# Kernel tuning notes

Hardware: AMD Instinct MI355X
Metric: run time of the kernel (lower is better)

Reference implementation:

```python
import jax, jax.numpy as jnp
import numpy as np

B, S, D = 4, 2048, 1024
LN_EPS = 1e-5
NEG_INF = -1e9


def _layernorm(x, gamma, beta):
    mu = jnp.mean(x, axis=-1, keepdims=True)
    var = jnp.var(x, axis=-1, keepdims=True)
    return (x - mu) * jax.lax.rsqrt(var + LN_EPS) * gamma + beta


def setup_inputs() -> dict:
    key = jax.random.key(0)
    k1, k2, k3, k4 = jax.random.split(key, 4)
    context = jax.random.normal(k1, (B, S, D), dtype=jnp.float32)
    eos_mask = jnp.ones((B, S, S), dtype=jnp.int64)
    prior = jax.random.uniform(k2, (B, S, S), dtype=jnp.float32)
    bound = 1.0 / np.sqrt(D)
    Wq = jax.random.uniform(k3, (D, D), dtype=jnp.float32, minval=-bound, maxval=bound)
    Wk = jax.random.uniform(k4, (D, D), dtype=jnp.float32, minval=-bound, maxval=bound)
    gamma = jnp.ones((D,), dtype=jnp.float32)
    beta = jnp.zeros((D,), dtype=jnp.float32)
    return {"context": context, "eos_mask": eos_mask, "prior": prior,
            "Wq": Wq, "Wk": Wk, "gamma": gamma, "beta": beta}


def reference(context, eos_mask, prior, Wq, Wk, gamma, beta):
    d_model = context.shape[-1]
    seq_len = context.shape[1]
    x = _layernorm(context, gamma, beta)
    q = x @ Wq.T                                   # nn.Linear, no bias
    k = x @ Wk.T
    scores = jnp.einsum('bsd,btd->bst', q, k) / jnp.sqrt(jnp.asarray(d_model, x.dtype))

    idx = jnp.arange(seq_len)
    a_sup = idx[:, None] + 1 == idx[None, :]       # superdiagonal (torch `a`)
    c_sub = idx[:, None] - 1 == idx[None, :]       # subdiagonal  (torch `c`)
    diag = idx[:, None] == idx[None, :]            # identity     (torch `b`)
    strict_lower = idx[:, None] > idx[None, :]     # tril - eye

    # mask = eos_mask & (a + c)  (Python precedence: & binds looser than +)
    mask = (eos_mask != 0) & (a_sup | c_sub)
    scores = jnp.where(mask, scores, NEG_INF)
    neibor_attn = jax.nn.softmax(scores, axis=-1)
    neibor_attn = jnp.sqrt(neibor_attn * jnp.swapaxes(neibor_attn, -1, -2) + 1e-9)
    neibor_attn = prior + (1.0 - prior) * neibor_attn

    # t = log(neibor+1e-9).masked_fill(a==0,0) @ tril  == reverse cumsum over last axis
    logn = jnp.where(a_sup, jnp.log(neibor_attn + 1e-9), 0.0)
    t = jnp.cumsum(logn[:, :, ::-1], axis=-1)[:, :, ::-1]
    # g = exp(tril @ t), keep strictly-lower part ((tril - eye) != 0)
    g = jnp.exp(jnp.cumsum(t, axis=1))
    g = jnp.where(strict_lower, g, 0.0)

    g_attn = g + jnp.swapaxes(g, -1, -2) + jnp.where(diag, neibor_attn, 1e-9)
    return g_attn, neibor_attn
```

## Files before the change

kernel.cpp:

```cpp
#include <hip/hip_runtime.h>
#include <hip/hip_bf16.h>
#include <stdint.h>

#define SS 2048
#define DD 1024
#define RR 8192

typedef _Float16 f16;
typedef _Float16 f16x8 __attribute__((ext_vector_type(8)));
typedef _Float16 f16x4 __attribute__((ext_vector_type(4)));
typedef float    f32x4 __attribute__((ext_vector_type(4)));

__device__ __forceinline__ void gl_lds16(const f16* g, f16* l) {
  __builtin_amdgcn_global_load_lds((const __attribute__((address_space(1))) void*)g,
                                   (__attribute__((address_space(3))) void*)l,
                                   16, 0, 0);
}

__global__ __launch_bounds__(256) void k_pre(const float* __restrict__ x,
                                             const float* __restrict__ gamma,
                                             const float* __restrict__ beta,
                                             f16* __restrict__ xn,
                                             const float* __restrict__ Wq,
                                             const float* __restrict__ Wk,
                                             f16* __restrict__ Wqt,
                                             f16* __restrict__ Wkt,
                                             const int* __restrict__ eos,
                                             const float* __restrict__ prior,
                                             float* __restrict__ sup_g,
                                             float* __restrict__ sub_g,
                                             int* __restrict__ e_sup,
                                             int* __restrict__ e_sub,
                                             float* __restrict__ pr_sup) {
  __shared__ f16 tile[64][72];
  int bidx = blockIdx.x;
  int t = threadIdx.x;
  if (bidx < RR) {
    int lane = t & 63, w = t >> 6;
    const float* xr = x + (size_t)bidx * DD;
    float4 v = ((const float4*)xr)[t];
    float s  = v.x + v.y + v.z + v.w;
    float ss = v.x*v.x + v.y*v.y + v.z*v.z + v.w*v.w;
#pragma unroll
    for (int off = 32; off > 0; off >>= 1) {
      s  += __shfl_down(s,  off, 64);
      ss += __shfl_down(ss, off, 64);
    }
    float* r0 = (float*)&tile[0][0];
    float* r1 = r0 + 4;
    if (lane == 0) { r0[w] = s; r1[w] = ss; }
    __syncthreads();
    float tot = r0[0]+r0[1]+r0[2]+r0[3];
    float tss = r1[0]+r1[1]+r1[2]+r1[3];
    float mu  = tot * (1.0f/DD);
    float var = tss * (1.0f/DD) - mu*mu;
    float inv = rsqrtf(var + 1e-5f);
    float4 g = ((const float4*)gamma)[t];
    float4 b = ((const float4*)beta)[t];
    f16x4 o;
    o[0] = (f16)((v.x-mu)*inv*g.x + b.x);
    o[1] = (f16)((v.y-mu)*inv*g.y + b.y);
    o[2] = (f16)((v.z-mu)*inv*g.z + b.z);
    o[3] = (f16)((v.w-mu)*inv*g.w + b.w);
    *(f16x4*)(xn + (size_t)bidx*DD + t*4) = o;
  } else if (bidx < RR + 512) {
    int bid = bidx - RR;
    const float* src = (bid & 1) ? Wk : Wq;
    f16* dst = (bid & 1) ? Wkt : Wqt;
    int tb = bid >> 1;
    int r0 = (tb >> 4) << 6, c0 = (tb & 15) << 6;
#pragma unroll
    for (int p = 0; p < 4; ++p) {
      int r = p * 16 + (t >> 4);
      int c = (t & 15) * 4;
      float4 v = *(const float4*)(src + (size_t)(r0 + r) * DD + c0 + c);
      tile[c + 0][r] = (f16)v.x; tile[c + 1][r] = (f16)v.y;
      tile[c + 2][r] = (f16)v.z; tile[c + 3][r] = (f16)v.w;
    }
    __syncthreads();
    int orow = t >> 2, och = (t & 3) * 16;
    f16x8 a = *(const f16x8*)&tile[orow][och];
    f16x8 b = *(const f16x8*)&tile[orow][och + 8];
    f16* o = dst + (size_t)(c0 + orow) * DD + r0 + och;
    *(f16x8*)o = a;
    *(f16x8*)(o + 8) = b;
  } else {
    int g = bidx - (RR + 512);
    int u = g * 256 + t;
    sup_g[u] = 0.f;
    sub_g[u] = 0.f;
    if (u < 4 * 2047) {
      int b = u / 2047;
      int s = u - b * 2047;
      size_t ebase = (size_t)b * SS * SS;
      int bS = b * SS;
      e_sup[bS + s]     = eos[ebase + (size_t)s * SS + s + 1];
      e_sub[bS + s + 1] = eos[ebase + (size_t)(s + 1) * SS + s];
      pr_sup[bS + s]    = prior[ebase + (size_t)s * SS + s + 1];
    }
  }
}

template<int BM, int BN, int LOG2NBN, bool FUSE>
__global__ __launch_bounds__(256) void k_gemm_t(const f16* __restrict__ A,
                                                const f16* __restrict__ Bw,
                                                f16* __restrict__ C,
                                                float* __restrict__ sup_g,
                                                float* __restrict__ sub_g) {
  constexpr int K  = 1024;
  constexpr int NC = 1024;
  constexpr int MF = BM / 32;
  constexpr int NF = BN / 32;
  constexpr int IA = BM / 64;
  constexpr int IB = BN / 64;
  constexpr int XST = 136;
  __shared__ f16 As[BM * 32];
  __shared__ f16 Bs[BN * 32];
  __shared__ f16 Xs[FUSE ? 130 * XST : 1];
  int cpx = gridDim.x >> 3;
  int bid = (blockIdx.x & 7) * cpx + (blockIdx.x >> 3);
  int bm = bid >> LOG2NBN, bn = bid & ((1 << LOG2NBN) - 1);
  int tid = threadIdx.x;
  int lane = tid & 63, w = tid >> 6;
  int wm = w >> 1, wn = w & 1;

  f32x4 acc[MF][NF] = {};

  int srow = w * 16 + (lane >> 2);
  int sch  = lane & 3;
  const f16* AgI[IA];
  const f16* BgI[IB];
  f16* lAI[IA];
  f16* lBI[IB];
#pragma unroll
  for (int i = 0; i < IA; ++i) {
    AgI[i] = A + (size_t)(bm * BM + i * 64 + srow) * K + sch * 8;
    lAI[i] = As + (i * 64 + w * 16) * 32;
  }
#pragma unroll
  for (int i = 0; i < IB; ++i) {
    BgI[i] = Bw + (size_t)(bn * BN + i * 64 + srow) * K + sch * 8;
    lBI[i] = Bs + (i * 64 + w * 16) * 32;
  }

  int rlo = lane & 15, rch = (lane >> 4) * 8;

  for (int kt = 0; kt < K; kt += 32) {
    __syncthreads();
#pragma unroll
    for (int i = 0; i < IA; ++i) gl_lds16(AgI[i] + kt, lAI[i]);
#pragma unroll
    for (int i = 0; i < IB; ++i) gl_lds16(BgI[i] + kt, lBI[i]);
    __syncthreads();
    f16x8 af[MF], bf[NF];
#pragma unroll
    for (int mi = 0; mi < MF; ++mi)
      af[mi] = *(const f16x8*)(As + (wm * (BM/2) + mi * 16 + rlo) * 32 + rch);
#pragma unroll
    for (int ni = 0; ni < NF; ++ni)
      bf[ni] = *(const f16x8*)(Bs + (wn * (BN/2) + ni * 16 + rlo) * 32 + rch);
#pragma unroll
    for (int mi = 0; mi < MF; ++mi)
#pragma unroll
      for (int ni = 0; ni < NF; ++ni)
        acc[mi][ni] = __builtin_amdgcn_mfma_f32_16x16x32_f16(af[mi], bf[ni], acc[mi][ni], 0, 0, 0);
  }
  int c0 = (lane >> 4) * 4;
  if constexpr (!FUSE) {
#pragma unroll
    for (int mi = 0; mi < MF; ++mi)
#pragma unroll
      for (int ni = 0; ni < NF; ++ni)
#pragma unroll
        for (int r = 0; r < 4; ++r) {
          int row = bm * BM + wm * (BM/2) + mi * 16 + c0 + r;
          int col = bn * BN + wn * (BN/2) + ni * 16 + rlo;
          C[(size_t)row * NC + col] = (f16)acc[mi][ni][r];
        }
  } else {
    int slabBase = bm * BM - 1;
#pragma unroll
    for (int it = 0; it < 9; ++it) {
      int c = tid + it * 256;
      if (c < 130 * 16) {
        int rI = c >> 4, colc = (c & 15) * 8;
        int gr = slabBase + rI;
        gr = gr < 0 ? 0 : (gr > RR - 1 ? RR - 1 : gr);
        *(f16x8*)(Xs + rI * XST + colc) =
            *(const f16x8*)(A + (size_t)gr * K + bn * BN + colc);
      }
    }
    __syncthreads();
#pragma unroll
    for (int mi = 0; mi < MF; ++mi) {
#pragma unroll
      for (int r = 0; r < 4; ++r) {
        int rloc = wm * (BM/2) + mi * 16 + c0 + r;
        float su = 0.f, sb = 0.f;
#pragma unroll
        for (int ni = 0; ni < NF; ++ni) {
          float y = acc[mi][ni][r];
          int colL = wn * (BN/2) + ni * 16 + rlo;
          su += y * (float)Xs[rloc * XST + colL];
          sb += y * (float)Xs[(rloc + 2) * XST + colL];
        }
#pragma unroll
        for (int m = 1; m < 16; m <<= 1) {
          su += __shfl_xor(su, m, 64);
          sb += __shfl_xor(sb, m, 64);
        }
        if (rlo == 0) {
          int rho = bm * BM + rloc;
          if ((rho & (SS - 1)) != 0)
            atomicAdd(&sup_g[rho - 1], su * 0.03125f);
          if ((rho & (SS - 1)) != SS - 1)
            atomicAdd(&sub_g[rho + 1], sb * 0.03125f);
        }
      }
    }
  }
}

__global__ __launch_bounds__(1024) void k_scan(const float* __restrict__ sup,
                                               const float* __restrict__ sub,
                                               const int* __restrict__ e_sup,
                                               const int* __restrict__ e_sub,
                                               const float* __restrict__ pr_sup,
                                               float* __restrict__ p_sup,
                                               float* __restrict__ p_sub,
                                               double* __restrict__ P) {
  int b = blockIdx.x, t = threadIdx.x;
  int lane = t & 63, wid = t >> 6;
  int bS = b * SS;
  __shared__ float  psub_sh[SS];
  __shared__ double wsum[16];
  float psup_loc[2];
#pragma unroll
  for (int e = 0; e < 2; ++e) {
    int s = 2*t + e;
    bool supOK = (s < SS-1) && (e_sup[bS + s] != 0);
    bool subOK = (s >= 1)   && (e_sub[bS + s] != 0);
    float ps = 0.f, pb = 0.f;
    if (supOK && subOK) {
      float Av = sup[bS + s], Cv = sub[bS + s];
      float m  = fmaxf(Av, Cv);
      float ea = expf(Av - m), eb = expf(Cv - m);
      float iv = 1.0f / (ea + eb);
      ps = ea * iv; pb = eb * iv;
    } else if (supOK) ps = 1.f;
    else if (subOK)   pb = 1.f;
    p_sup[bS + s] = ps; p_sub[bS + s] = pb;
    psub_sh[s] = pb; psup_loc[e] = ps;
  }
  __syncthreads();
  double L0 = 0.0, L1 = 0.0;
#pragma unroll
  for (int e = 0; e < 2; ++e) {
    int s = 2*t + e;
    double Lv = 0.0;
    if (s < SS-1) {
      float pr = pr_sup[bS + s];
      float vv = sqrtf(psup_loc[e] * psub_sh[s+1] + 1e-9f);
      Lv = (double)logf(pr + (1.f - pr)*vv + 1e-9f);
    }
    if (e == 0) L0 = Lv; else L1 = Lv;
  }
  double pairv = L0 + L1;
  double v = pairv;
#pragma unroll
  for (int off = 1; off < 64; off <<= 1) {
    double u = __shfl_up(v, off, 64);
    if (lane >= off) v += u;
  }
  if (lane == 63) wsum[wid] = v;
  __syncthreads();
  double base = 0.0;
  for (int wI = 0; wI < wid; ++wI) base += wsum[wI];
  double excl = base + v - pairv;
  P[bS + 2*t]     = excl + L0;
  P[bS + 2*t + 1] = excl + L0 + L1;
}

__global__ __launch_bounds__(256) void k_out(const float* __restrict__ prior,
                                             const float* __restrict__ p_sup,
                                             const float* __restrict__ p_sub,
                                             const double* __restrict__ P,
                                             float* __restrict__ g_out,
                                             float* __restrict__ n_out) {
  size_t v = (size_t)blockIdx.x * 256 + threadIdx.x;
  int j4   = (int)(v & 511);
  int rowg = (int)(v >> 9);
  int s = rowg & (SS - 1);
  int b = rowg >> 11;
  size_t base = (size_t)rowg * SS + j4 * 4;
  union F4 { float4 v4; float a[4]; };
  F4 prf; prf.v4 = *(const float4*)(prior + base);
  int bS = b * SS;
  double Ps  = P[bS + s];
  double Ps2 = (s >= 2) ? P[bS + s - 2] : 0.0;
  const float SQ9 = 3.1622776601683795e-5f;
  F4 gv, nv;
#pragma unroll
  for (int e = 0; e < 4; ++e) {
    int j = j4*4 + e;
    float pr = prf.a[e];
    float vv;
    if (j == s + 1)      vv = sqrtf(p_sup[bS+s] * p_sub[bS+s+1] + 1e-9f);
    else if (j == s - 1) vv = sqrtf(p_sub[bS+s] * p_sup[bS+s-1] + 1e-9f);
    else                 vv = SQ9;
    float na = pr + (1.f - pr) * vv;
    nv.a[e] = na;
    float g;
    if (s == j) g = na;
    else if (s > j) {
      double Pj2 = (j >= 2) ? P[bS + j - 2] : 0.0;
      g = expf((float)(Ps - Pj2)) + 1e-9f;
    } else {
      g = expf((float)(P[bS + j] - Ps2)) + 1e-9f;
    }
    gv.a[e] = g;
  }
  *(float4*)(g_out + base) = gv.v4;
  *(float4*)(n_out + base) = nv.v4;
}

extern "C" void kernel_launch(void* const* d_in, const int* in_sizes, int n_in,
                              void* d_out, int out_size, void* d_ws, size_t ws_size,
                              hipStream_t stream) {
  const float* context = (const float*)d_in[0];
  const int*   eos     = (const int*)d_in[1];
  const float* prior   = (const float*)d_in[2];
  const float* Wq      = (const float*)d_in[3];
  const float* Wk      = (const float*)d_in[4];
  const float* gamma   = (const float*)d_in[5];
  const float* beta    = (const float*)d_in[6];

  char* ws = (char*)d_ws;
  float*  sup    = (float*)(ws);
  float*  sub    = (float*)(ws + 32768);
  float*  p_sup  = (float*)(ws + 65536);
  float*  p_sub  = (float*)(ws + 98304);
  double* P      = (double*)(ws + 131072);
  int*    e_sup  = (int*)(ws + 196608);
  int*    e_sub  = (int*)(ws + 229376);
  float*  pr_sup = (float*)(ws + 262144);
  const size_t smallEnd = 294912;

  const size_t XN_BYTES = (size_t)RR * DD * 2;
  const size_t WT_BYTES = (size_t)DD * DD * 2;
  const size_t bigNeed  = XN_BYTES + 3 * WT_BYTES;
  char* big;
  if (ws_size >= smallEnd + bigNeed) big = ws + smallEnd;
  else big = (char*)d_out + ((size_t)out_size * 4 - bigNeed);
  f16* Xn  = (f16*)big;
  f16* Wqt = (f16*)(big + XN_BYTES);
  f16* Wkt = (f16*)(big + XN_BYTES + WT_BYTES);
  f16* Mm  = (f16*)(big + XN_BYTES + 2 * WT_BYTES);

  k_pre<<<RR + 512 + 32, 256, 0, stream>>>(context, gamma, beta, Xn, Wq, Wk, Wqt, Wkt,
                                           eos, prior, sup, sub, e_sup, e_sub, pr_sup);
  k_gemm_t<64, 64, 4, false><<<256, 256, 0, stream>>>(Wqt, Wkt, Mm, nullptr, nullptr);
  k_gemm_t<128, 128, 3, true><<<512, 256, 0, stream>>>(Xn, Mm, nullptr, sup, sub);
  k_scan<<<4, 1024, 0, stream>>>(sup, sub, e_sup, e_sub, pr_sup, p_sup, p_sub, P);
  float* g_out = (float*)d_out;
  float* n_out = g_out + (size_t)RR * SS;
  k_out<<<16384, 256, 0, stream>>>(prior, p_sup, p_sub, P, g_out, n_out);
}
```

Measured before the change: 105.1 us.

## Fuse scan into Y-GEMM via last-block counter and double-buffer M-GEMM loads

```diff
diff --git a/kernel.cpp b/kernel.cpp
--- a/kernel.cpp
+++ b/kernel.cpp
@@ -15,6 +15,10 @@
   __builtin_amdgcn_global_load_lds((const __attribute__((address_space(1))) void*)g,
                                    (__attribute__((address_space(3))) void*)l,
                                    16, 0, 0);
+}
+
+__device__ __forceinline__ float loada(const float* p) {
+  return __hip_atomic_load(p, __ATOMIC_RELAXED, __HIP_MEMORY_SCOPE_AGENT);
 }
 
 __global__ __launch_bounds__(256) void k_pre(const float* __restrict__ x,
@@ -31,7 +35,8 @@
                                              float* __restrict__ sub_g,
                                              int* __restrict__ e_sup,
                                              int* __restrict__ e_sub,
-                                             float* __restrict__ pr_sup) {
+                                             float* __restrict__ pr_sup,
+                                             unsigned* __restrict__ ctr) {
   __shared__ f16 tile[64][72];
   int bidx = blockIdx.x;
   int t = threadIdx.x;
@@ -87,6 +92,7 @@
   } else {
     int g = bidx - (RR + 512);
     int u = g * 256 + t;
+    if (u == 0) *ctr = 0u;
     sup_g[u] = 0.f;
     sub_g[u] = 0.f;
     if (u < 4 * 2047) {
@@ -101,184 +107,225 @@
   }
 }
 
-template<int BM, int BN, int LOG2NBN, bool FUSE>
-__global__ __launch_bounds__(256) void k_gemm_t(const f16* __restrict__ A,
-                                                const f16* __restrict__ Bw,
-                                                f16* __restrict__ C,
-                                                float* __restrict__ sup_g,
-                                                float* __restrict__ sub_g) {
-  constexpr int K  = 1024;
-  constexpr int NC = 1024;
-  constexpr int MF = BM / 32;
-  constexpr int NF = BN / 32;
-  constexpr int IA = BM / 64;
-  constexpr int IB = BN / 64;
-  constexpr int XST = 136;
-  __shared__ f16 As[BM * 32];
-  __shared__ f16 Bs[BN * 32];
-  __shared__ f16 Xs[FUSE ? 130 * XST : 1];
-  int cpx = gridDim.x >> 3;
-  int bid = (blockIdx.x & 7) * cpx + (blockIdx.x >> 3);
-  int bm = bid >> LOG2NBN, bn = bid & ((1 << LOG2NBN) - 1);
+__global__ __launch_bounds__(256) void k_mgemm(const f16* __restrict__ A,
+                                               const f16* __restrict__ Bw,
+                                               f16* __restrict__ C) {
+  constexpr int K = 1024;
+  __shared__ f16 As[2][64 * 32];
+  __shared__ f16 Bs[2][64 * 32];
+  int cpx = (int)gridDim.x >> 3;
+  int bid = ((int)blockIdx.x & 7) * cpx + ((int)blockIdx.x >> 3);
+  int bm = bid >> 4, bn = bid & 15;
   int tid = threadIdx.x;
   int lane = tid & 63, w = tid >> 6;
   int wm = w >> 1, wn = w & 1;
-
-  f32x4 acc[MF][NF] = {};
+  f32x4 acc[2][2] = {};
 
   int srow = w * 16 + (lane >> 2);
   int sch  = lane & 3;
-  const f16* AgI[IA];
-  const f16* BgI[IB];
-  f16* lAI[IA];
-  f16* lBI[IB];
-#pragma unroll
-  for (int i = 0; i < IA; ++i) {
-    AgI[i] = A + (size_t)(bm * BM + i * 64 + srow) * K + sch * 8;
-    lAI[i] = As + (i * 64 + w * 16) * 32;
-  }
-#pragma unroll
-  for (int i = 0; i < IB; ++i) {
-    BgI[i] = Bw + (size_t)(bn * BN + i * 64 + srow) * K + sch * 8;
-    lBI[i] = Bs + (i * 64 + w * 16) * 32;
-  }
-
+  const f16* Ag = A  + (size_t)(bm * 64 + srow) * K + sch * 8;
+  const f16* Bg = Bw + (size_t)(bn * 64 + srow) * K + sch * 8;
+  f16* lA = &As[0][0] + w * 16 * 32;
+  f16* lB = &Bs[0][0] + w * 16 * 32;
   int rlo = lane & 15, rch = (lane >> 4) * 8;
 
-  for (int kt = 0; kt < K; kt += 32) {
-    __syncthreads();
-#pragma unroll
-    for (int i = 0; i < IA; ++i) gl_lds16(AgI[i] + kt, lAI[i]);
-#pragma unroll
-    for (int i = 0; i < IB; ++i) gl_lds16(BgI[i] + kt, lBI[i]);
-    __syncthreads();
-    f16x8 af[MF], bf[NF];
-#pragma unroll
-    for (int mi = 0; mi < MF; ++mi)
-      af[mi] = *(const f16x8*)(As + (wm * (BM/2) + mi * 16 + rlo) * 32 + rch);
-#pragma unroll
-    for (int ni = 0; ni < NF; ++ni)
-      bf[ni] = *(const f16x8*)(Bs + (wn * (BN/2) + ni * 16 + rlo) * 32 + rch);
-#pragma unroll
-    for (int mi = 0; mi < MF; ++mi)
-#pragma unroll
-      for (int ni = 0; ni < NF; ++ni)
+  gl_lds16(Ag, lA);
+  gl_lds16(Bg, lB);
+  for (int t = 0; t < 32; ++t) {
+    int cur = t & 1;
+    __syncthreads();
+    if (t < 31) {
+      gl_lds16(Ag + (t + 1) * 32, lA + (cur ^ 1) * 64 * 32);
+      gl_lds16(Bg + (t + 1) * 32, lB + (cur ^ 1) * 64 * 32);
+    }
+    f16x8 af[2], bf[2];
+#pragma unroll
+    for (int mi = 0; mi < 2; ++mi)
+      af[mi] = *(const f16x8*)(&As[cur][(wm * 32 + mi * 16 + rlo) * 32 + rch]);
+#pragma unroll
+    for (int ni = 0; ni < 2; ++ni)
+      bf[ni] = *(const f16x8*)(&Bs[cur][(wn * 32 + ni * 16 + rlo) * 32 + rch]);
+#pragma unroll
+    for (int mi = 0; mi < 2; ++mi)
+#pragma unroll
+      for (int ni = 0; ni < 2; ++ni)
         acc[mi][ni] = __builtin_amdgcn_mfma_f32_16x16x32_f16(af[mi], bf[ni], acc[mi][ni], 0, 0, 0);
   }
   int c0 = (lane >> 4) * 4;
-  if constexpr (!FUSE) {
-#pragma unroll
-    for (int mi = 0; mi < MF; ++mi)
-#pragma unroll
-      for (int ni = 0; ni < NF; ++ni)
-#pragma unroll
-        for (int r = 0; r < 4; ++r) {
-          int row = bm * BM + wm * (BM/2) + mi * 16 + c0 + r;
-          int col = bn * BN + wn * (BN/2) + ni * 16 + rlo;
-          C[(size_t)row * NC + col] = (f16)acc[mi][ni][r];
-        }
-  } else {
-    int slabBase = bm * BM - 1;
-#pragma unroll
-    for (int it = 0; it < 9; ++it) {
-      int c = tid + it * 256;
-      if (c < 130 * 16) {
-        int rI = c >> 4, colc = (c & 15) * 8;
-        int gr = slabBase + rI;
-        gr = gr < 0 ? 0 : (gr > RR - 1 ? RR - 1 : gr);
-        *(f16x8*)(Xs + rI * XST + colc) =
-            *(const f16x8*)(A + (size_t)gr * K + bn * BN + colc);
+#pragma unroll
+  for (int mi = 0; mi < 2; ++mi)
+#pragma unroll
+    for (int ni = 0; ni < 2; ++ni)
+#pragma unroll
+      for (int r = 0; r < 4; ++r) {
+        int row = bm * 64 + wm * 32 + mi * 16 + c0 + r;
+        int col = bn * 64 + wn * 32 + ni * 16 + rlo;
+        C[(size_t)row * DD + col] = (f16)acc[mi][ni][r];
       }
-    }
-    __syncthreads();
-#pragma unroll
-    for (int mi = 0; mi < MF; ++mi) {
-#pragma unroll
-      for (int r = 0; r < 4; ++r) {
-        int rloc = wm * (BM/2) + mi * 16 + c0 + r;
-        float su = 0.f, sb = 0.f;
-#pragma unroll
-        for (int ni = 0; ni < NF; ++ni) {
-          float y = acc[mi][ni][r];
-          int colL = wn * (BN/2) + ni * 16 + rlo;
-          su += y * (float)Xs[rloc * XST + colL];
-          sb += y * (float)Xs[(rloc + 2) * XST + colL];
-        }
-#pragma unroll
-        for (int m = 1; m < 16; m <<= 1) {
-          su += __shfl_xor(su, m, 64);
-          sb += __shfl_xor(sb, m, 64);
-        }
-        if (rlo == 0) {
-          int rho = bm * BM + rloc;
-          if ((rho & (SS - 1)) != 0)
-            atomicAdd(&sup_g[rho - 1], su * 0.03125f);
-          if ((rho & (SS - 1)) != SS - 1)
-            atomicAdd(&sub_g[rho + 1], sb * 0.03125f);
-        }
-      }
-    }
-  }
-}
-
-__global__ __launch_bounds__(1024) void k_scan(const float* __restrict__ sup,
-                                               const float* __restrict__ sub,
+}
+
+__global__ __launch_bounds__(256) void k_ygemm(const f16* __restrict__ A,
+                                               const f16* __restrict__ Bw,
+                                               float* __restrict__ sup_g,
+                                               float* __restrict__ sub_g,
                                                const int* __restrict__ e_sup,
                                                const int* __restrict__ e_sub,
                                                const float* __restrict__ pr_sup,
                                                float* __restrict__ p_sup,
                                                float* __restrict__ p_sub,
-                                               double* __restrict__ P) {
-  int b = blockIdx.x, t = threadIdx.x;
-  int lane = t & 63, wid = t >> 6;
-  int bS = b * SS;
-  __shared__ float  psub_sh[SS];
-  __shared__ double wsum[16];
-  float psup_loc[2];
-#pragma unroll
-  for (int e = 0; e < 2; ++e) {
-    int s = 2*t + e;
-    bool supOK = (s < SS-1) && (e_sup[bS + s] != 0);
-    bool subOK = (s >= 1)   && (e_sub[bS + s] != 0);
-    float ps = 0.f, pb = 0.f;
-    if (supOK && subOK) {
-      float Av = sup[bS + s], Cv = sub[bS + s];
-      float m  = fmaxf(Av, Cv);
-      float ea = expf(Av - m), eb = expf(Cv - m);
-      float iv = 1.0f / (ea + eb);
-      ps = ea * iv; pb = eb * iv;
-    } else if (supOK) ps = 1.f;
-    else if (subOK)   pb = 1.f;
-    p_sup[bS + s] = ps; p_sub[bS + s] = pb;
-    psub_sh[s] = pb; psup_loc[e] = ps;
+                                               double* __restrict__ P,
+                                               unsigned* __restrict__ ctr) {
+  constexpr int K = 1024, BM = 128, BN = 128;
+  constexpr int XST = 136;
+  __shared__ f16 As[BM * 32];
+  __shared__ f16 Bs[BN * 32];
+  __shared__ f16 Xs[130 * XST];
+  __shared__ int lastFlag;
+  int cpx = (int)gridDim.x >> 3;
+  int bid = ((int)blockIdx.x & 7) * cpx + ((int)blockIdx.x >> 3);
+  int bm = bid >> 3, bn = bid & 7;
+  int tid = threadIdx.x;
+  int lane = tid & 63, w = tid >> 6;
+  int wm = w >> 1, wn = w & 1;
+
+  f32x4 acc[4][4] = {};
+
+  int srow = w * 16 + (lane >> 2);
+  int sch  = lane & 3;
+  const f16* Ag0 = A  + (size_t)(bm * BM + srow) * K + sch * 8;
+  const f16* Ag1 = Ag0 + (size_t)64 * K;
+  const f16* Bg0 = Bw + (size_t)(bn * BN + srow) * K + sch * 8;
+  const f16* Bg1 = Bg0 + (size_t)64 * K;
+  f16* lA0 = As + (w * 16) * 32;
+  f16* lA1 = As + (64 + w * 16) * 32;
+  f16* lB0 = Bs + (w * 16) * 32;
+  f16* lB1 = Bs + (64 + w * 16) * 32;
+  int rlo = lane & 15, rch = (lane >> 4) * 8;
+
+  for (int kt = 0; kt < K; kt += 32) {
+    __syncthreads();
+    gl_lds16(Ag0 + kt, lA0);
+    gl_lds16(Ag1 + kt, lA1);
+    gl_lds16(Bg0 + kt, lB0);
+    gl_lds16(Bg1 + kt, lB1);
+    __syncthreads();
+    f16x8 af[4], bf[4];
+#pragma unroll
+    for (int mi = 0; mi < 4; ++mi)
+      af[mi] = *(const f16x8*)(As + (wm * 64 + mi * 16 + rlo) * 32 + rch);
+#pragma unroll
+    for (int ni = 0; ni < 4; ++ni)
+      bf[ni] = *(const f16x8*)(Bs + (wn * 64 + ni * 16 + rlo) * 32 + rch);
+#pragma unroll
+    for (int mi = 0; mi < 4; ++mi)
+#pragma unroll
+      for (int ni = 0; ni < 4; ++ni)
+        acc[mi][ni] = __builtin_amdgcn_mfma_f32_16x16x32_f16(af[mi], bf[ni], acc[mi][ni], 0, 0, 0);
+  }
+  int c0 = (lane >> 4) * 4;
+  int slabBase = bm * BM - 1;
+#pragma unroll
+  for (int it = 0; it < 9; ++it) {
+    int c = tid + it * 256;
+    if (c < 130 * 16) {
+      int rI = c >> 4, colc = (c & 15) * 8;
+      int gr = slabBase + rI;
+      gr = gr < 0 ? 0 : (gr > RR - 1 ? RR - 1 : gr);
+      *(f16x8*)(Xs + rI * XST + colc) =
+          *(const f16x8*)(A + (size_t)gr * K + bn * BN + colc);
+    }
   }
   __syncthreads();
-  double L0 = 0.0, L1 = 0.0;
-#pragma unroll
-  for (int e = 0; e < 2; ++e) {
-    int s = 2*t + e;
-    double Lv = 0.0;
-    if (s < SS-1) {
-      float pr = pr_sup[bS + s];
-      float vv = sqrtf(psup_loc[e] * psub_sh[s+1] + 1e-9f);
-      Lv = (double)logf(pr + (1.f - pr)*vv + 1e-9f);
-    }
-    if (e == 0) L0 = Lv; else L1 = Lv;
-  }
-  double pairv = L0 + L1;
-  double v = pairv;
-#pragma unroll
-  for (int off = 1; off < 64; off <<= 1) {
-    double u = __shfl_up(v, off, 64);
-    if (lane >= off) v += u;
-  }
-  if (lane == 63) wsum[wid] = v;
+#pragma unroll
+  for (int mi = 0; mi < 4; ++mi) {
+#pragma unroll
+    for (int r = 0; r < 4; ++r) {
+      int rloc = wm * 64 + mi * 16 + c0 + r;
+      float su = 0.f, sb = 0.f;
+#pragma unroll
+      for (int ni = 0; ni < 4; ++ni) {
+        float y = acc[mi][ni][r];
+        int colL = wn * 64 + ni * 16 + rlo;
+        su += y * (float)Xs[rloc * XST + colL];
+        sb += y * (float)Xs[(rloc + 2) * XST + colL];
+      }
+#pragma unroll
+      for (int m = 1; m < 16; m <<= 1) {
+        su += __shfl_xor(su, m, 64);
+        sb += __shfl_xor(sb, m, 64);
+      }
+      if (rlo == 0) {
+        int rho = bm * BM + rloc;
+        if ((rho & (SS - 1)) != 0)
+          atomicAdd(&sup_g[rho - 1], su * 0.03125f);
+        if ((rho & (SS - 1)) != SS - 1)
+          atomicAdd(&sub_g[rho + 1], sb * 0.03125f);
+      }
+    }
+  }
   __syncthreads();
-  double base = 0.0;
-  for (int wI = 0; wI < wid; ++wI) base += wsum[wI];
-  double excl = base + v - pairv;
-  P[bS + 2*t]     = excl + L0;
-  P[bS + 2*t + 1] = excl + L0 + L1;
+  if (tid == 0) {
+    __threadfence();
+    unsigned r = atomicAdd(ctr, 1u);
+    lastFlag = (r == gridDim.x - 1) ? 1 : 0;
+  }
+  __syncthreads();
+  if (!lastFlag) return;
+  __threadfence();
+
+  float*  psubF = (float*)As;
+  double* wsumD = (double*)Bs;
+  for (int b = 0; b < 4; ++b) {
+    int bS = b * SS;
+    __syncthreads();
+    float psl[8], pbl[8];
+#pragma unroll
+    for (int e = 0; e < 8; ++e) {
+      int s = tid * 8 + e;
+      bool supOK = (s < SS - 1) && (e_sup[bS + s] != 0);
+      bool subOK = (s >= 1) && (e_sub[bS + s] != 0);
+      float ps = 0.f, pb = 0.f;
+      if (supOK && subOK) {
+        float Av = loada(&sup_g[bS + s]), Cv = loada(&sub_g[bS + s]);
+        float m  = fmaxf(Av, Cv);
+        float ea = expf(Av - m), eb = expf(Cv - m);
+        float iv = 1.0f / (ea + eb);
+        ps = ea * iv; pb = eb * iv;
+      } else if (supOK) ps = 1.f;
+      else if (subOK)   pb = 1.f;
+      p_sup[bS + s] = ps; p_sub[bS + s] = pb;
+      psl[e] = ps; pbl[e] = pb;
+    }
+    psubF[tid] = pbl[0];
+    __syncthreads();
+    float pbn = (tid < 255) ? psubF[tid + 1] : 0.f;
+    double pre[8]; double run = 0.0;
+#pragma unroll
+    for (int e = 0; e < 8; ++e) {
+      int s = tid * 8 + e;
+      if (s < SS - 1) {
+        float pnx = (e < 7) ? pbl[e + 1] : pbn;
+        float vv = sqrtf(psl[e] * pnx + 1e-9f);
+        float pr = pr_sup[bS + s];
+        run += (double)logf(pr + (1.f - pr) * vv + 1e-9f);
+      }
+      pre[e] = run;
+    }
+    double tot = run, v = run;
+    int lane2 = tid & 63, wv = tid >> 6;
+#pragma unroll
+    for (int off = 1; off < 64; off <<= 1) {
+      double u = __shfl_up(v, off, 64);
+      if (lane2 >= off) v += u;
+    }
+    if (lane2 == 63) wsumD[wv] = v;
+    __syncthreads();
+    double base = 0.0;
+    for (int w2 = 0; w2 < wv; ++w2) base += wsumD[w2];
+    double excl = base + v - tot;
+#pragma unroll
+    for (int e = 0; e < 8; ++e) P[bS + tid * 8 + e] = excl + pre[e];
+  }
 }
 
 __global__ __launch_bounds__(256) void k_out(const float* __restrict__ prior,
@@ -336,15 +383,16 @@
   const float* beta    = (const float*)d_in[6];
 
   char* ws = (char*)d_ws;
-  float*  sup    = (float*)(ws);
-  float*  sub    = (float*)(ws + 32768);
-  float*  p_sup  = (float*)(ws + 65536);
-  float*  p_sub  = (float*)(ws + 98304);
-  double* P      = (double*)(ws + 131072);
-  int*    e_sup  = (int*)(ws + 196608);
-  int*    e_sub  = (int*)(ws + 229376);
-  float*  pr_sup = (float*)(ws + 262144);
-  const size_t smallEnd = 294912;
+  float*    sup    = (float*)(ws);
+  float*    sub    = (float*)(ws + 32768);
+  float*    p_sup  = (float*)(ws + 65536);
+  float*    p_sub  = (float*)(ws + 98304);
+  double*   P      = (double*)(ws + 131072);
+  int*      e_sup  = (int*)(ws + 196608);
+  int*      e_sub  = (int*)(ws + 229376);
+  float*    pr_sup = (float*)(ws + 262144);
+  unsigned* ctr    = (unsigned*)(ws + 294912);
+  const size_t smallEnd = 294928;
 
   const size_t XN_BYTES = (size_t)RR * DD * 2;
   const size_t WT_BYTES = (size_t)DD * DD * 2;
@@ -358,10 +406,10 @@
   f16* Mm  = (f16*)(big + XN_BYTES + 2 * WT_BYTES);
 
   k_pre<<<RR + 512 + 32, 256, 0, stream>>>(context, gamma, beta, Xn, Wq, Wk, Wqt, Wkt,
-                                           eos, prior, sup, sub, e_sup, e_sub, pr_sup);
-  k_gemm_t<64, 64, 4, false><<<256, 256, 0, stream>>>(Wqt, Wkt, Mm, nullptr, nullptr);
-  k_gemm_t<128, 128, 3, true><<<512, 256, 0, stream>>>(Xn, Mm, nullptr, sup, sub);
-  k_scan<<<4, 1024, 0, stream>>>(sup, sub, e_sup, e_sub, pr_sup, p_sup, p_sub, P);
+                                           eos, prior, sup, sub, e_sup, e_sub, pr_sup, ctr);
+  k_mgemm<<<256, 256, 0, stream>>>(Wqt, Wkt, Mm);
+  k_ygemm<<<512, 256, 0, stream>>>(Xn, Mm, sup, sub, e_sup, e_sub, pr_sup,
+                                   p_sup, p_sub, P, ctr);
   float* g_out = (float*)d_out;
   float* n_out = g_out + (size_t)RR * SS;
   k_out<<<16384, 256, 0, stream>>>(prior, p_sup, p_sub, P, g_out, n_out);
```

Measured after the change: 154.5 us. +47.0%, slower.
